# Performance work log

Hardware: AMD Instinct MI355X
Metric: run time of the kernel (lower is better)

The kernel has to match this reference:

```python
import jax, jax.numpy as jnp
import numpy as np

N_NODES = 30000
N_REL = 8
N_EDGES = 150000
EMB = 128
HID = 128
OUT = 256
HEADS = 4
RANK = 8
SCALE = 1.0
NEG_SLOPE = 0.2
LN_EPS = 1e-5


def setup_inputs():
    key = jax.random.key(0)
    ks = jax.random.split(key, 16)
    def nrm(k, shp, s=0.05):
        return jax.random.normal(k, shp, dtype=jnp.float32) * s
    d2 = HEADS * HID  # conv2 input dim = 512
    return {
        "entity_emb": nrm(ks[0], (N_NODES, EMB)),
        "A1": nrm(ks[1], (N_REL, EMB * RANK)),
        "B1": nrm(ks[2], (N_REL, EMB * RANK)),
        "W1": nrm(ks[3], (HEADS * HID, EMB)),
        "att_l1": nrm(ks[4], (1, HEADS, HID)),
        "att_r1": nrm(ks[5], (1, HEADS, HID)),
        "relb1": jnp.zeros((N_REL, HEADS), jnp.float32),
        "bias1": jnp.zeros((HEADS * HID,), jnp.float32),
        "A2": nrm(ks[6], (N_REL, d2 * RANK)),
        "B2": nrm(ks[7], (N_REL, d2 * RANK)),
        "W2": nrm(ks[8], (OUT, d2)),
        "att_l2": nrm(ks[9], (1, 1, OUT)),
        "att_r2": nrm(ks[10], (1, 1, OUT)),
        "relb2": jnp.zeros((N_REL, 1), jnp.float32),
        "bias2": jnp.zeros((OUT,), jnp.float32),
        "res_W": nrm(ks[11], (OUT, EMB)),
        "res_b": jnp.zeros((OUT,), jnp.float32),
        "ln_g": jnp.ones((OUT,), jnp.float32),
        "ln_b": jnp.zeros((OUT,), jnp.float32),
        "edge_index": jax.random.randint(ks[12], (2, N_EDGES), 0, N_NODES),
        "edge_type": jax.random.randint(ks[13], (N_EDGES,), 0, N_REL),
    }


def _rel_gat_conv(x, A, B, W, att_l, att_r, relb, bias, j_idx, i_idx, etype, heads, out_dim, concat):
    # x: [N,d]; A,B: [R, d*k]; W: [heads*out_dim, d]
    N, d = x.shape
    R = A.shape[0]
    k = RANK
    HC = heads * out_dim
    A3 = A.reshape(R, d, k)
    B3 = B.reshape(R, d, k)
    z_all = x @ W.T  # [N, HC] base linear (shared by z_i and z_j)
    # LoRA low-rank projection per (node, relation): P[n,r] = B_r^T x_n
    P = jnp.einsum('nd,rdk->nrk', x, B3)          # [N,R,k] (small)
    low = P[j_idx, etype]                          # [E,k]
    # Fused LoRA-through-lin: lin(scale*A_r B_r^T x) = scale * low @ (A_r^T W^T)
    M = jnp.einsum('rdk,hd->rkh', A3, W).reshape(R * k, HC)  # [R*k, HC]
    oh = jax.nn.one_hot(etype, R, dtype=x.dtype)   # [E,R]
    low_exp = (oh[:, :, None] * low[:, None, :]).reshape(-1, R * k)  # [E,R*k]
    z_j = (z_all[j_idx] + SCALE * (low_exp @ M)).reshape(-1, heads, out_dim)  # [E,H,C]
    z_i = z_all[i_idx].reshape(-1, heads, out_dim)                            # [E,H,C]
    alpha = (z_i * att_l).sum(-1) + (z_j * att_r).sum(-1) + relb[etype]       # [E,H]
    alpha = jax.nn.leaky_relu(alpha, NEG_SLOPE)
    # per-relation loop => softmax groups are (relation, target node)
    seg = etype * N + i_idx
    n_seg = R * N
    amax = jax.ops.segment_max(alpha, seg, num_segments=n_seg)
    ex = jnp.exp(alpha - amax[seg])
    den = jax.ops.segment_sum(ex, seg, num_segments=n_seg)
    alpha = ex / den[seg]
    msg = z_j * alpha[:, :, None]                  # [E,H,C]
    out = jax.ops.segment_sum(msg, i_idx, num_segments=N)  # [N,H,C]
    out = out.reshape(N, HC) if concat else out.mean(axis=1)
    return out + bias


def _forward(entity_emb, A1, B1, W1, att_l1, att_r1, relb1, bias1,
             A2, B2, W2, att_l2, att_r2, relb2, bias2,
             res_W, res_b, ln_g, ln_b, edge_index, edge_type):
    j_idx, i_idx = edge_index[0], edge_index[1]
    x0 = entity_emb
    x = _rel_gat_conv(x0, A1, B1, W1, att_l1, att_r1, relb1, bias1,
                      j_idx, i_idx, edge_type, HEADS, HID, True)
    x = jax.nn.elu(x)
    x = _rel_gat_conv(x, A2, B2, W2, att_l2, att_r2, relb2, bias2,
                      j_idx, i_idx, edge_type, 1, OUT, False)
    x = x + (x0 @ res_W.T + res_b)
    mu = x.mean(axis=-1, keepdims=True)
    var = ((x - mu) ** 2).mean(axis=-1, keepdims=True)
    return (x - mu) / jnp.sqrt(var + LN_EPS) * ln_g + ln_b


def reference(entity_emb, A1, B1, W1, att_l1, att_r1, relb1, bias1,
              A2, B2, W2, att_l2, att_r2, relb2, bias2,
              res_W, res_b, ln_g, ln_b, edge_index, edge_type):
    return _forward(entity_emb, A1, B1, W1, att_l1, att_r1, relb1, bias1,
                    A2, B2, W2, att_l2, att_r2, relb2, bias2,
                    res_W, res_b, ln_g, ln_b, edge_index, edge_type)
```

## Files before the change

kernel.cpp:

```cpp
#include <hip/hip_runtime.h>
#include <cstddef>

#define NRELS 8
#define EMB 128
#define HID 128
#define OUTD 256
#define HEADS 4
#define RANK 8
#define D2 512
#define KCAT 192
#define NEG_SLOPE 0.2f
#define LN_EPS 1e-5f

typedef short bf16x8 __attribute__((ext_vector_type(8)));
typedef float f32x4 __attribute__((ext_vector_type(4)));

__device__ __forceinline__ unsigned short f2bf(float f) {
  union { float f; unsigned u; } v; v.f = f;
  unsigned u = v.u;
  return (unsigned short)((u + 0x7fffu + ((u >> 16) & 1u)) >> 16);
}
__device__ __forceinline__ float bf2f(unsigned short u) {
  union { unsigned u; float f; } v; v.u = (unsigned)u << 16; return v.f;
}

#define GLOAD16(ldsp, gp) \
  __builtin_amdgcn_global_load_lds((const __attribute__((address_space(1))) unsigned int*)(gp), \
      (__attribute__((address_space(3))) unsigned int*)(ldsp), 16, 0, 0)

template<int BIAS, int F32OUT, int ELU, int PB>
__global__ __launch_bounds__(256) void gemm_tile(const unsigned short* __restrict__ A,
    const unsigned short* __restrict__ B, unsigned short* __restrict__ C,
    float* __restrict__ Cf, const unsigned short* __restrict__ Bp,
    float* __restrict__ Cp, int M, int N, int K, int lda, int aoffc,
    const float* __restrict__ bias, const float* __restrict__ b1p) {
  __shared__ unsigned short As[2][128 * 32];
  __shared__ unsigned short Bs[2][128 * 32];
  const int tid = threadIdx.x;
  const int wave = tid >> 6;
  const int lane = tid & 63;
  const int wm = wave & 1;
  const int wn = wave >> 1;
  const int r16 = lane & 15;
  const int quad = lane >> 4;
  const int bm = blockIdx.x * 128;
  const int lr = lane >> 2;
  const int lc = ((lane & 3) ^ ((lane >> 3) & 3)) * 8;
  const int rsw = (quad ^ ((r16 >> 1) & 3)) * 8;
  const bool isP = PB && (blockIdx.y == (int)gridDim.y - 1);
  const unsigned short* Bu = isP ? Bp : B;
  const int bn = isP ? 0 : blockIdx.y * 128;
  const unsigned short* Abase = A + (size_t)blockIdx.y * (isP ? 0 : aoffc);
  int ar0 = bm + wave * 32 + lr;      if (ar0 >= M) ar0 = M - 1;
  int ar1 = bm + wave * 32 + 16 + lr; if (ar1 >= M) ar1 = M - 1;
  const unsigned short* Ag0 = Abase + (size_t)ar0 * lda + lc;
  const unsigned short* Ag1 = Abase + (size_t)ar1 * lda + lc;
  const unsigned short* Bg0 = Bu + (size_t)(bn + wave * 32 + lr) * K + lc;
  const unsigned short* Bg1 = Bu + (size_t)(bn + wave * 32 + 16 + lr) * K + lc;
  f32x4 acc[4][4] = {};
  GLOAD16(As[0] + wave * 1024, Ag0);
  GLOAD16(As[0] + wave * 1024 + 512, Ag1);
  GLOAD16(Bs[0] + wave * 1024, Bg0);
  GLOAD16(Bs[0] + wave * 1024 + 512, Bg1);
  __syncthreads();
  int cur = 0;
  for (int k0 = 0; k0 < K; k0 += 32) {
    if (k0 + 32 < K) {
      GLOAD16(As[cur ^ 1] + wave * 1024, Ag0 + k0 + 32);
      GLOAD16(As[cur ^ 1] + wave * 1024 + 512, Ag1 + k0 + 32);
      GLOAD16(Bs[cur ^ 1] + wave * 1024, Bg0 + k0 + 32);
      GLOAD16(Bs[cur ^ 1] + wave * 1024 + 512, Bg1 + k0 + 32);
    }
    bf16x8 af[4], bfr[4];
#pragma unroll
    for (int mi = 0; mi < 4; ++mi)
      af[mi] = *(const bf16x8*)(As[cur] + (wm * 64 + mi * 16 + r16) * 32 + rsw);
#pragma unroll
    for (int ni = 0; ni < 4; ++ni)
      bfr[ni] = *(const bf16x8*)(Bs[cur] + (wn * 64 + ni * 16 + r16) * 32 + rsw);
#pragma unroll
    for (int mi = 0; mi < 4; ++mi)
#pragma unroll
      for (int ni = 0; ni < 4; ++ni)
        acc[mi][ni] = __builtin_amdgcn_mfma_f32_16x16x32_bf16(af[mi], bfr[ni], acc[mi][ni], 0, 0, 0);
    __syncthreads();
    cur ^= 1;
  }
  float bcol[4];
  if (BIAS) {
#pragma unroll
    for (int ni = 0; ni < 4; ++ni) {
      int cn = bn + wn * 64 + ni * 16 + r16;
      bcol[ni] = bias[cn];
      if (F32OUT) bcol[ni] += b1p[cn];
    }
  }
#pragma unroll
  for (int mi = 0; mi < 4; ++mi)
#pragma unroll
    for (int ni = 0; ni < 4; ++ni)
#pragma unroll
      for (int r = 0; r < 4; ++r) {
        int row = bm + wm * 64 + mi * 16 + quad * 4 + r;
        if (row < M) {
          int col = wn * 64 + ni * 16 + r16;
          float v = acc[mi][ni][r];
          if (isP) {
            Cp[(size_t)row * 128 + col] = v;
          } else {
            if (BIAS) v += bcol[ni];
            if (ELU) v = v > 0.f ? v : expm1f(v);
            size_t idx = (size_t)row * N + bn + col;
            if (F32OUT) Cf[idx] = v;
            else        C[idx] = f2bf(v);
          }
        }
      }
}

__global__ __launch_bounds__(256) void gemm_abt2(const float* __restrict__ Amat1,
    const float* __restrict__ W1, float* __restrict__ M1o,
    const float* __restrict__ Amat2, const float* __restrict__ W2, float* __restrict__ M2o) {
  const float* A; const float* B; float* C; int N, K, bn;
  if (blockIdx.x < D2 / 64) { A = Amat1; B = W1; C = M1o; N = D2; K = EMB; bn = blockIdx.x * 64; }
  else { A = Amat2; B = W2; C = M2o; N = OUTD; K = D2; bn = (blockIdx.x - D2 / 64) * 64; }
  __shared__ float As[32][64];
  __shared__ float Bs[32][64];
  const int tid = threadIdx.x;
  const int tx = tid & 15;
  const int ty = tid >> 4;
  const int lr = tid & 63;
  const int lq = tid >> 6;
  float acc[4][4] = {};
  for (int k0 = 0; k0 < K; k0 += 32) {
#pragma unroll
    for (int s = 0; s < 2; ++s) {
      const int q = lq + s * 4;
      float4 va = *(const float4*)(A + (size_t)lr * K + k0 + q * 4);
      As[q * 4 + 0][lr] = va.x; As[q * 4 + 1][lr] = va.y;
      As[q * 4 + 2][lr] = va.z; As[q * 4 + 3][lr] = va.w;
      float4 vb = *(const float4*)(B + (size_t)(bn + lr) * K + k0 + q * 4);
      Bs[q * 4 + 0][lr] = vb.x; Bs[q * 4 + 1][lr] = vb.y;
      Bs[q * 4 + 2][lr] = vb.z; Bs[q * 4 + 3][lr] = vb.w;
    }
    __syncthreads();
#pragma unroll
    for (int kk = 0; kk < 32; ++kk) {
      float a[4], b[4];
#pragma unroll
      for (int i2 = 0; i2 < 4; ++i2) { a[i2] = As[kk][ty * 4 + i2]; b[i2] = Bs[kk][tx * 4 + i2]; }
#pragma unroll
      for (int i2 = 0; i2 < 4; ++i2)
#pragma unroll
        for (int j2 = 0; j2 < 4; ++j2)
          acc[i2][j2] = fmaf(a[i2], b[j2], acc[i2][j2]);
    }
    __syncthreads();
  }
#pragma unroll
  for (int i2 = 0; i2 < 4; ++i2)
#pragma unroll
    for (int j2 = 0; j2 < 4; ++j2)
      C[(size_t)(ty * 4 + i2) * N + bn + tx * 4 + j2] = acc[i2][j2];
}

__global__ void prep_all(const float* __restrict__ x0, const float* __restrict__ W2,
    const float* __restrict__ res_W,
    const float* __restrict__ A1, const float* __restrict__ A2,
    const float* __restrict__ B1, const float* __restrict__ B2,
    unsigned short* __restrict__ x0b, unsigned short* __restrict__ Acat,
    unsigned short* __restrict__ W2b, unsigned short* __restrict__ RWcat,
    float* __restrict__ Amat1, float* __restrict__ Amat2,
    unsigned short* __restrict__ Bmat1b, unsigned short* __restrict__ Bmat2b,
    const int* __restrict__ ii, int* __restrict__ ideg, int* __restrict__ prepos,
    int E, int nx0) {
  int idx = blockIdx.x * 256 + threadIdx.x;
  if (idx < E) { prepos[idx] = atomicAdd(&ideg[ii[idx]], 1); return; } idx -= E;
  if (idx < nx0) { unsigned short b = f2bf(x0[idx]); x0b[idx] = b;
    Acat[(size_t)(idx >> 7) * KCAT + (idx & 127)] = b; return; } idx -= nx0;
  if (idx < OUTD * D2) { W2b[idx] = f2bf(W2[idx]); return; } idx -= OUTD * D2;
  if (idx < OUTD * EMB) { RWcat[(size_t)(idx >> 7) * KCAT + (idx & 127)] = f2bf(res_W[idx]); return; } idx -= OUTD * EMB;
  if (idx < 64 * EMB) { int d = idx % EMB, rk = idx / EMB, k = rk & 7, r = rk >> 3;
    Amat1[idx] = A1[(size_t)r * EMB * RANK + (size_t)d * RANK + k]; return; } idx -= 64 * EMB;
  if (idx < 64 * D2) { int d = idx % D2, rk = idx / D2, k = rk & 7, r = rk >> 3;
    Amat2[idx] = A2[(size_t)r * D2 * RANK + (size_t)d * RANK + k]; return; } idx -= 64 * D2;
  if (idx < 64 * EMB) { int d = idx % EMB, rk = idx / EMB, k = rk & 7, r = rk >> 3;
    Bmat1b[idx] = f2bf(B1[(size_t)r * EMB * RANK + (size_t)d * RANK + k]); return; } idx -= 64 * EMB;
  if (idx < 64 * D2) { int d = idx % D2, rk = idx / D2, k = rk & 7, r = rk >> 3;
    Bmat2b[idx] = f2bf(B2[(size_t)r * D2 * RANK + (size_t)d * RANK + k]); }
}

__global__ void fold_build(const float* __restrict__ M1, const float* __restrict__ M2,
    const float* __restrict__ W1, const float* __restrict__ W2,
    const float* __restrict__ attL1, const float* __restrict__ attR1,
    const float* __restrict__ attL2, const float* __restrict__ attR2,
    const unsigned short* __restrict__ Bmat1b, const unsigned short* __restrict__ Bmat2b,
    unsigned short* __restrict__ Bcat1, unsigned short* __restrict__ RWcat,
    unsigned short* __restrict__ Bp1ext, unsigned short* __restrict__ Bp2ext,
    float* __restrict__ Matt1, float* __restrict__ Matt2) {
  int idx = blockIdx.x * 256 + threadIdx.x;
  if (idx < 512 * 192) { int c = idx / 192, t = idx % 192;
    float v = (t < 128) ? W1[(size_t)c * EMB + t] : M1[(size_t)(t - 128) * D2 + c];
    Bcat1[idx] = f2bf(v); return; } idx -= 512 * 192;
  if (idx < 256 * 64) { int c = idx >> 6, rk = idx & 63;
    RWcat[(size_t)c * KCAT + 128 + rk] = f2bf(M2[(size_t)rk * OUTD + c]); return; } idx -= 256 * 64;
  if (idx < 128 * 128) { int r = idx >> 7, d = idx & 127;
    unsigned short v;
    if (r < 64) v = Bmat1b[r * 128 + d];
    else if (r < 72) { int h = (r - 64) & 3;
      const float* att = (r < 68) ? attL1 : attR1;
      float s = 0.f;
      for (int c = 0; c < HID; ++c)
        s = fmaf(W1[(size_t)(h * HID + c) * EMB + d], att[h * HID + c], s);
      v = f2bf(s); }
    else v = 0;
    Bp1ext[idx] = v; return; } idx -= 128 * 128;
  if (idx < 128 * 512) { int r = idx >> 9, d = idx & 511;
    unsigned short v;
    if (r < 64) v = Bmat2b[r * 512 + d];
    else if (r < 66) { const float* att = (r == 64) ? attL2 : attR2;
      float s = 0.f;
      for (int c = 0; c < OUTD; ++c)
        s = fmaf(W2[(size_t)c * D2 + d], att[c], s);
      v = f2bf(s); }
    else v = 0;
    Bp2ext[idx] = v; return; } idx -= 128 * 512;
  if (idx < 256) { int h = idx & 3, rk = idx >> 2;
    float s = 0.f;
    for (int c = 0; c < HID; ++c)
      s = fmaf(M1[(size_t)rk * D2 + h * HID + c], attR1[h * HID + c], s);
    Matt1[rk * 4 + h] = s; return; } idx -= 256;
  if (idx < 64) {
    float s = 0.f;
    for (int c = 0; c < OUTD; ++c) s = fmaf(M2[(size_t)idx * OUTD + c], attR2[c], s);
    Matt2[idx] = s; }
}

__global__ __launch_bounds__(1024) void exscan_kernel(const int* __restrict__ deg,
                                                      int* __restrict__ rowstart, int n) {
  __shared__ int wsum[16];
  int t = threadIdx.x;
  int lane = t & 63, wid = t >> 6;
  int carry = 0;
  for (int base = 0; base < n; base += 4096) {
    int i0 = base + t * 4;
    int v0 = 0, v1 = 0, v2 = 0, v3 = 0;
    if (i0 + 3 < n) {
      int4 vv = *(const int4*)(deg + i0);
      v0 = vv.x; v1 = vv.y; v2 = vv.z; v3 = vv.w;
    } else {
      if (i0 < n) v0 = deg[i0];
      if (i0 + 1 < n) v1 = deg[i0 + 1];
      if (i0 + 2 < n) v2 = deg[i0 + 2];
      if (i0 + 3 < n) v3 = deg[i0 + 3];
    }
    int tot = v0 + v1 + v2 + v3;
    int x = tot;
#pragma unroll
    for (int o = 1; o < 64; o <<= 1) {
      int y = __shfl_up(x, o, 64);
      if (lane >= o) x += y;
    }
    if (lane == 63) wsum[wid] = x;
    __syncthreads();
    if (t == 0) {
      int s = carry;
      for (int w2 = 0; w2 < 16; ++w2) { int tmp = wsum[w2]; wsum[w2] = s; s += tmp; }
      carry = s;
    }
    __syncthreads();
    int ex0 = x - tot + wsum[wid];
    if (i0 + 3 < n) {
      int4 ov; ov.x = ex0; ov.y = ex0 + v0; ov.z = ex0 + v0 + v1; ov.w = ex0 + v0 + v1 + v2;
      *(int4*)(rowstart + i0) = ov;
    } else {
      if (i0 < n) rowstart[i0] = ex0;
      if (i0 + 1 < n) rowstart[i0 + 1] = ex0 + v0;
      if (i0 + 2 < n) rowstart[i0 + 2] = ex0 + v0 + v1;
      if (i0 + 3 < n) rowstart[i0 + 3] = ex0 + v0 + v1 + v2;
    }
    __syncthreads();
  }
  if (t == 0) rowstart[n] = carry;
}

__global__ void edge_alpha1(const int* __restrict__ ji, const int* __restrict__ ii,
                            const int* __restrict__ et, const int* __restrict__ rowstart,
                            const int* __restrict__ prepos,
                            const float* __restrict__ Cp1,
                            const float* __restrict__ relb1, const float* __restrict__ Matt1,
                            float4* __restrict__ recs1, int E) {
  int e = blockIdx.x * blockDim.x + threadIdx.x;
  if (e >= E) return;
  int j = ji[e], i = ii[e], rt = et[e];
  float4 lo0 = *(const float4*)(Cp1 + (size_t)j * 128 + rt * 8);
  float4 lo1 = *(const float4*)(Cp1 + (size_t)j * 128 + rt * 8 + 4);
  float low[RANK] = {lo0.x, lo0.y, lo0.z, lo0.w, lo1.x, lo1.y, lo1.z, lo1.w};
  float4 ali = *(const float4*)(Cp1 + (size_t)i * 128 + 64);
  float4 arj = *(const float4*)(Cp1 + (size_t)j * 128 + 68);
  float4 rb  = *(const float4*)(relb1 + rt * 4);
  float a0 = ali.x + arj.x + rb.x;
  float a1 = ali.y + arj.y + rb.y;
  float a2 = ali.z + arj.z + rb.z;
  float a3 = ali.w + arj.w + rb.w;
#pragma unroll
  for (int k = 0; k < RANK; ++k) {
    float4 mk = *(const float4*)(Matt1 + ((rt * 8 + k) << 2));
    a0 = fmaf(low[k], mk.x, a0); a1 = fmaf(low[k], mk.y, a1);
    a2 = fmaf(low[k], mk.z, a2); a3 = fmaf(low[k], mk.w, a3);
  }
  a0 = (a0 > 0.f) ? a0 : NEG_SLOPE * a0;
  a1 = (a1 > 0.f) ? a1 : NEG_SLOPE * a1;
  a2 = (a2 > 0.f) ? a2 : NEG_SLOPE * a2;
  a3 = (a3 > 0.f) ? a3 : NEG_SLOPE * a3;
  float e0 = expf(a0), e1 = expf(a1), e2 = expf(a2), e3 = expf(a3);
  float4* rp = recs1 + (size_t)(rowstart[i] + prepos[e]) * 4;
  rp[0] = make_float4(__int_as_float(j), e0, e1, e2);
  rp[1] = make_float4(e3, __int_as_float(rt), low[0], low[1]);
  rp[2] = make_float4(low[2], low[3], low[4], low[5]);
  rp[3] = make_float4(low[6], low[7], 0.f, 0.f);
}

__global__ __launch_bounds__(256) void agg1f(const float4* __restrict__ recs1,
    const int* __restrict__ rowstart, const unsigned short* __restrict__ x0b,
    unsigned short* __restrict__ XQ1, int Nn) {
  __shared__ float denS[4][32];
  const int wid = threadIdx.x >> 6, lane = threadIdx.x & 63;
  const int i = blockIdx.x * 4 + wid;
  if (i >= Nn) return;
  const int rt_mine = lane >> 3, k = lane & 7;
  const int s0 = rowstart[i], deg = rowstart[i + 1] - s0;
  const float* rf = (const float*)recs1;
  const size_t xb = (size_t)i * 768;
  {
    float q0 = 0.f, q1 = 0.f, q2 = 0.f, q3 = 0.f;
    float d0 = 0.f, d1 = 0.f, d2 = 0.f, d3 = 0.f;
    float4 a0 = {}, a1 = {};
    float lw = 0.f;
    if (deg > 0) {
      a0 = recs1[(size_t)s0 * 4]; a1 = recs1[(size_t)s0 * 4 + 1];
      lw = rf[(size_t)s0 * 16 + 6 + k];
    }
    for (int p = 0; p < deg; ++p) {
      float4 b0 = a0, b1 = a1; float lwn = lw;
      if (p + 1 < deg) {
        b0 = recs1[(size_t)(s0 + p + 1) * 4]; b1 = recs1[(size_t)(s0 + p + 1) * 4 + 1];
        lwn = rf[(size_t)(s0 + p + 1) * 16 + 6 + k];
      }
      int rt = __float_as_int(a1.y);
      if (rt == rt_mine) {
        q0 = fmaf(a0.y, lw, q0); q1 = fmaf(a0.z, lw, q1);
        q2 = fmaf(a0.w, lw, q2); q3 = fmaf(a1.x, lw, q3);
        d0 += a0.y; d1 += a0.z; d2 += a0.w; d3 += a1.x;
      }
      a0 = b0; a1 = b1; lw = lwn;
    }
    float r0 = (d0 > 0.f) ? 1.f / d0 : 0.f;
    float r1 = (d1 > 0.f) ? 1.f / d1 : 0.f;
    float r2 = (d2 > 0.f) ? 1.f / d2 : 0.f;
    float r3 = (d3 > 0.f) ? 1.f / d3 : 0.f;
    XQ1[xb + 0 * 192 + 128 + lane] = f2bf(q0 * r0);
    XQ1[xb + 1 * 192 + 128 + lane] = f2bf(q1 * r1);
    XQ1[xb + 2 * 192 + 128 + lane] = f2bf(q2 * r2);
    XQ1[xb + 3 * 192 + 128 + lane] = f2bf(q3 * r3);
    if (k == 0) {
      denS[wid][rt_mine]      = r0;
      denS[wid][8 + rt_mine]  = r1;
      denS[wid][16 + rt_mine] = r2;
      denS[wid][24 + rt_mine] = r3;
    }
  }
  const int c0 = lane * 2;
  float acc[8] = {};
  float4 r0 = {}, r1 = {};
  float2 g0 = {}, g1 = {};
  unsigned za = 0u, zn0 = 0u;
  if (deg > 0) { r0 = recs1[(size_t)s0 * 4]; g0 = *(const float2*)(rf + (size_t)s0 * 16 + 4);
    za = *(const unsigned*)(x0b + (size_t)__float_as_int(r0.x) * 128 + c0); }
  if (deg > 1) { r1 = recs1[(size_t)(s0 + 1) * 4]; g1 = *(const float2*)(rf + (size_t)(s0 + 1) * 16 + 4); }
  for (int p = 0; p < deg; ++p) {
    float4 r2 = r1; float2 g2 = g1; unsigned zb = za;
    if (p + 2 < deg) { r2 = recs1[(size_t)(s0 + p + 2) * 4];
                       g2 = *(const float2*)(rf + (size_t)(s0 + p + 2) * 16 + 4); }
    if (p + 1 < deg) zb = *(const unsigned*)(x0b + (size_t)__float_as_int(r1.x) * 128 + c0);
    int rt = __float_as_int(g0.y);
    float w0 = r0.y * denS[wid][rt];
    float w1 = r0.z * denS[wid][8 + rt];
    float w2 = r0.w * denS[wid][16 + rt];
    float w3 = g0.x * denS[wid][24 + rt];
    float v0 = bf2f((unsigned short)(za & 0xffff));
    float v1 = bf2f((unsigned short)(za >> 16));
    acc[0] = fmaf(w0, v0, acc[0]); acc[1] = fmaf(w0, v1, acc[1]);
    acc[2] = fmaf(w1, v0, acc[2]); acc[3] = fmaf(w1, v1, acc[3]);
    acc[4] = fmaf(w2, v0, acc[4]); acc[5] = fmaf(w2, v1, acc[5]);
    acc[6] = fmaf(w3, v0, acc[6]); acc[7] = fmaf(w3, v1, acc[7]);
    r0 = r1; g0 = g1; r1 = r2; g1 = g2; za = zb;
  }
#pragma unroll
  for (int h = 0; h < 4; ++h) {
    unsigned pv = (unsigned)f2bf(acc[2 * h]) | ((unsigned)f2bf(acc[2 * h + 1]) << 16);
    *(unsigned*)(XQ1 + xb + h * 192 + c0) = pv;
  }
}

__global__ void edge_alpha2(const int* __restrict__ ji, const int* __restrict__ ii,
                            const int* __restrict__ et, const int* __restrict__ rowstart,
                            const int* __restrict__ prepos,
                            const float* __restrict__ Cp2,
                            const float* __restrict__ relb2, const float* __restrict__ Matt2,
                            float4* __restrict__ recs2, int E) {
  int e = blockIdx.x * blockDim.x + threadIdx.x;
  if (e >= E) return;
  int j = ji[e], i = ii[e], rt = et[e];
  float4 lo0 = *(const float4*)(Cp2 + (size_t)j * 128 + rt * 8);
  float4 lo1 = *(const float4*)(Cp2 + (size_t)j * 128 + rt * 8 + 4);
  float low[RANK] = {lo0.x, lo0.y, lo0.z, lo0.w, lo1.x, lo1.y, lo1.z, lo1.w};
  float a = Cp2[(size_t)i * 128 + 64] + Cp2[(size_t)j * 128 + 65] + relb2[rt];
#pragma unroll
  for (int k = 0; k < RANK; ++k) a = fmaf(low[k], Matt2[rt * RANK + k], a);
  a = (a > 0.f) ? a : NEG_SLOPE * a;
  float ex = expf(a);
  float4* rp = recs2 + (size_t)(rowstart[i] + prepos[e]) * 3;
  rp[0] = make_float4(__int_as_float(j), __int_as_float(rt), ex, low[0]);
  rp[1] = make_float4(low[1], low[2], low[3], low[4]);
  rp[2] = make_float4(low[5], low[6], low[7], 0.f);
}

__global__ __launch_bounds__(256) void qden2(const float4* __restrict__ recs2,
    const int* __restrict__ rowstart, unsigned short* __restrict__ Acat,
    float* __restrict__ rden2, int Nn) {
  const int wid = threadIdx.x >> 6, lane = threadIdx.x & 63;
  const int i = blockIdx.x * 4 + wid;
  if (i >= Nn) return;
  const int rt_mine = lane >> 3, k = lane & 7;
  const int s0 = rowstart[i], deg = rowstart[i + 1] - s0;
  const float* rf = (const float*)recs2;
  float q = 0.f, d = 0.f;
  float4 a0 = {}; float lw = 0.f;
  if (deg > 0) { a0 = recs2[(size_t)s0 * 3]; lw = rf[(size_t)s0 * 12 + 3 + k]; }
  for (int p = 0; p < deg; ++p) {
    float4 b0 = a0; float lwn = lw;
    if (p + 1 < deg) {
      b0 = recs2[(size_t)(s0 + p + 1) * 3];
      lwn = rf[(size_t)(s0 + p + 1) * 12 + 3 + k];
    }
    int rt = __float_as_int(a0.y);
    if (rt == rt_mine) { q = fmaf(a0.z, lw, q); d += a0.z; }
    a0 = b0; lw = lwn;
  }
  float rd = (d > 0.f) ? 1.f / d : 0.f;
  Acat[(size_t)i * KCAT + 128 + lane] = f2bf(q * rd);
  if (k == 0) rden2[(size_t)i * 8 + rt_mine] = rd;
}

__global__ __launch_bounds__(256) void node_agg2_lite(const float4* __restrict__ recs2,
    const int* __restrict__ rowstart, const unsigned short* __restrict__ z2b,
    const float* __restrict__ rden2, const float* __restrict__ o2,
    const float* __restrict__ ln_g, const float* __restrict__ ln_b,
    float* __restrict__ y, int Nn) {
  const int wid = threadIdx.x >> 6;
  const int lane = threadIdx.x & 63;
  const int i = blockIdx.x * 4 + wid;
  if (i >= Nn) return;
  __shared__ float denS[4][NRELS];
  if (lane < NRELS) denS[wid][lane] = rden2[(size_t)i * 8 + lane];
  const int s0 = rowstart[i];
  const int deg = rowstart[i + 1] - s0;
  const int c0 = lane * 4;
  float acc[4] = {};
  float4 r0 = {}, r1 = {}, r2 = {};
  uint2 za = make_uint2(0u, 0u), zb = make_uint2(0u, 0u);
  if (deg > 0) { r0 = recs2[(size_t)s0 * 3];
    za = *(const uint2*)(z2b + (size_t)__float_as_int(r0.x) * OUTD + c0); }
  if (deg > 1) { r1 = recs2[(size_t)(s0 + 1) * 3];
    zb = *(const uint2*)(z2b + (size_t)__float_as_int(r1.x) * OUTD + c0); }
  if (deg > 2) r2 = recs2[(size_t)(s0 + 2) * 3];
  for (int p = 0; p < deg; ++p) {
    float4 r3 = r2;
    uint2 zn = zb;
    if (p + 3 < deg) r3 = recs2[(size_t)(s0 + p + 3) * 3];
    if (p + 2 < deg)
      zn = *(const uint2*)(z2b + (size_t)__float_as_int(r2.x) * OUTD + c0);
    int rt = __float_as_int(r0.y);
    float wt = r0.z * denS[wid][rt];
    acc[0] = fmaf(wt, bf2f((unsigned short)(za.x & 0xffff)), acc[0]);
    acc[1] = fmaf(wt, bf2f((unsigned short)(za.x >> 16)), acc[1]);
    acc[2] = fmaf(wt, bf2f((unsigned short)(za.y & 0xffff)), acc[2]);
    acc[3] = fmaf(wt, bf2f((unsigned short)(za.y >> 16)), acc[3]);
    r0 = r1; r1 = r2; r2 = r3; za = zb; zb = zn;
  }
  float4 rsv = *(const float4*)(o2 + (size_t)i * OUTD + c0);
  float vv[4];
  vv[0] = acc[0] + rsv.x;
  vv[1] = acc[1] + rsv.y;
  vv[2] = acc[2] + rsv.z;
  vv[3] = acc[3] + rsv.w;
  float s = vv[0] + vv[1] + vv[2] + vv[3];
  for (int o = 32; o > 0; o >>= 1) s += __shfl_xor(s, o, 64);
  float mu = s * (1.f / OUTD);
  float q = 0.f;
#pragma unroll
  for (int k = 0; k < 4; ++k) { float d = vv[k] - mu; q += d * d; }
  for (int o = 32; o > 0; o >>= 1) q += __shfl_xor(q, o, 64);
  float rstd = rsqrtf(q * (1.f / OUTD) + LN_EPS);
  float4 g = *(const float4*)(ln_g + c0);
  float4 bb = *(const float4*)(ln_b + c0);
  float4 ov;
  ov.x = (vv[0] - mu) * rstd * g.x + bb.x;
  ov.y = (vv[1] - mu) * rstd * g.y + bb.y;
  ov.z = (vv[2] - mu) * rstd * g.z + bb.z;
  ov.w = (vv[3] - mu) * rstd * g.w + bb.w;
  *(float4*)(y + (size_t)i * OUTD + c0) = ov;
}

extern "C" void kernel_launch(void* const* d_in, const int* in_sizes, int n_in,
                              void* d_out, int out_size, void* d_ws, size_t ws_size,
                              hipStream_t stream) {
  const float* x0     = (const float*)d_in[0];
  const float* A1     = (const float*)d_in[1];
  const float* B1     = (const float*)d_in[2];
  const float* W1     = (const float*)d_in[3];
  const float* attL1  = (const float*)d_in[4];
  const float* attR1  = (const float*)d_in[5];
  const float* relb1  = (const float*)d_in[6];
  const float* bias1  = (const float*)d_in[7];
  const float* A2     = (const float*)d_in[8];
  const float* B2     = (const float*)d_in[9];
  const float* W2     = (const float*)d_in[10];
  const float* attL2  = (const float*)d_in[11];
  const float* attR2  = (const float*)d_in[12];
  const float* relb2  = (const float*)d_in[13];
  const float* bias2  = (const float*)d_in[14];
  const float* res_W  = (const float*)d_in[15];
  const float* res_b  = (const float*)d_in[16];
  const float* ln_g   = (const float*)d_in[17];
  const float* ln_b   = (const float*)d_in[18];
  const int*   eidx   = (const int*)d_in[19];
  const int*   etype  = (const int*)d_in[20];
  float* out = (float*)d_out;

  const int Nn = in_sizes[0] / EMB;
  const int E  = in_sizes[20];
  const int* ji = eidx;
  const int* ii = eidx + E;

  float* w = (float*)d_ws;
  size_t off = 0;
  float* o2    = w + off; off += (size_t)Nn * OUTD;
  float* Cp1   = w + off; off += (size_t)Nn * 128;
  float* Cp2   = w + off; off += (size_t)Nn * 128;
  float* M1    = w + off; off += 64 * D2;
  float* M2    = w + off; off += 64 * OUTD;
  float* Amat1 = w + off; off += 64 * EMB;
  float* Amat2 = w + off; off += 64 * D2;
  float* Matt1 = w + off; off += 64 * 4;
  float* Matt2 = w + off; off += 64;
  float* rden2 = w + off; off += (size_t)Nn * 8;
  float4* recs1 = (float4*)(w + off); off += (size_t)E * 16;
  float4* recs2 = (float4*)(w + off); off += (size_t)E * 12;
  unsigned short* z2b    = (unsigned short*)(w + off); off += (size_t)Nn * OUTD / 2;
  unsigned short* x0b    = (unsigned short*)(w + off); off += (size_t)Nn * EMB / 2;
  unsigned short* h1b    = (unsigned short*)(w + off); off += (size_t)Nn * D2 / 2;
  unsigned short* XQ1    = (unsigned short*)(w + off); off += (size_t)Nn * 768 / 2;
  unsigned short* W2b    = (unsigned short*)(w + off); off += (size_t)OUTD * D2 / 2;
  unsigned short* Bmat1b = (unsigned short*)(w + off); off += (size_t)64 * EMB / 2;
  unsigned short* Bmat2b = (unsigned short*)(w + off); off += (size_t)64 * D2 / 2;
  unsigned short* Acat   = (unsigned short*)(w + off); off += (size_t)Nn * KCAT / 2;
  unsigned short* RWcat  = (unsigned short*)(w + off); off += (size_t)OUTD * KCAT / 2;
  unsigned short* Bcat1  = (unsigned short*)(w + off); off += (size_t)512 * 192 / 2;
  unsigned short* Bp1ext = (unsigned short*)(w + off); off += (size_t)128 * 128 / 2;
  unsigned short* Bp2ext = (unsigned short*)(w + off); off += (size_t)128 * 512 / 2;
  int* ideg     = (int*)(w + off); off += (size_t)Nn;
  int* prepos   = (int*)(w + off); off += (size_t)E;
  int* rowstart = (int*)(w + off); off += (size_t)Nn + 1;
  (void)ws_size; (void)n_in; (void)out_size;

  const int MT128 = (Nn + 127) / 128;
  const int NB4 = (Nn + 3) / 4;

  (void)hipMemsetAsync(ideg, 0, (size_t)Nn * sizeof(int), stream);
  {
    int nx0 = Nn * EMB;
    int total = E + nx0 + OUTD * D2 + OUTD * EMB + 64 * EMB + 64 * D2 + 64 * EMB + 64 * D2;
    prep_all<<<(total + 255) / 256, 256, 0, stream>>>(x0, W2, res_W, A1, A2, B1, B2,
        x0b, Acat, W2b, RWcat, Amat1, Amat2, Bmat1b, Bmat2b, ii, ideg, prepos, E, nx0);
  }
  exscan_kernel<<<1, 1024, 0, stream>>>(ideg, rowstart, Nn);

  gemm_abt2<<<dim3(D2 / 64 + OUTD / 64, 1), 256, 0, stream>>>(Amat1, W1, M1, Amat2, W2, M2);
  {
    int total = 512 * 192 + 256 * 64 + 128 * 128 + 128 * 512 + 256 + 64;
    fold_build<<<(total + 255) / 256, 256, 0, stream>>>(M1, M2, W1, W2, attL1, attR1,
        attL2, attR2, Bmat1b, Bmat2b, Bcat1, RWcat, Bp1ext, Bp2ext, Matt1, Matt2);
  }

  gemm_tile<0, 1, 0, 0><<<dim3(MT128, 1), 256, 0, stream>>>(x0b, Bp1ext, nullptr, Cp1,
      nullptr, nullptr, Nn, 128, EMB, EMB, 0, nullptr, nullptr);

  edge_alpha1<<<(E + 255) / 256, 256, 0, stream>>>(ji, ii, etype, rowstart, prepos, Cp1,
                                                   relb1, Matt1, recs1, E);
  agg1f<<<NB4, 256, 0, stream>>>(recs1, rowstart, x0b, XQ1, Nn);
  gemm_tile<1, 0, 1, 0><<<dim3(MT128, 4), 256, 0, stream>>>(XQ1, Bcat1, h1b, nullptr,
      nullptr, nullptr, Nn, D2, 192, 768, 192, bias1, nullptr);

  gemm_tile<0, 0, 0, 1><<<dim3(MT128, 3), 256, 0, stream>>>(h1b, W2b, z2b, nullptr,
      Bp2ext, Cp2, Nn, OUTD, D2, D2, 0, nullptr, nullptr);

  edge_alpha2<<<(E + 255) / 256, 256, 0, stream>>>(ji, ii, etype, rowstart, prepos, Cp2,
                                                   relb2, Matt2, recs2, E);
  qden2<<<NB4, 256, 0, stream>>>(recs2, rowstart, Acat, rden2, Nn);
  gemm_tile<1, 1, 0, 0><<<dim3(MT128, 2), 256, 0, stream>>>(Acat, RWcat, nullptr, o2,
      nullptr, nullptr, Nn, OUTD, KCAT, KCAT, 0, bias2, res_b);
  node_agg2_lite<<<NB4, 256, 0, stream>>>(recs2, rowstart, z2b, rden2, o2, ln_g, ln_b, out, Nn);
}
```

Measured before the change: 341.5 us.

## Merge prep-stage kernels and pack edge records into bf16 compact format

Several small setup kernels are folded into fewer launches. The weight-fold GEMM now runs alongside the x0 projection GEMM in one grid, the fold-build runs alongside edge_alpha1, and the Matt computation runs inside the scan kernel, now reassociated as Amat·(W^T att). Edge records are repacked: relation type and source index share one word, and the low-rank values are stored as bf16 pairs, which shrinks recs1 and recs2. This is meant to cut launch count and edge-record memory traffic, at the cost of lower precision on the LoRA terms and extra unpack work in the gather loops.

Result: no change. 341.1 us (-0.1%).

```diff
diff --git a/kernel.cpp b/kernel.cpp
--- a/kernel.cpp
+++ b/kernel.cpp
@@ -11,6 +11,7 @@
 #define KCAT 192
 #define NEG_SLOPE 0.2f
 #define LN_EPS 1e-5f
+#define JMASK 0x07FFFFFFu
 
 typedef short bf16x8 __attribute__((ext_vector_type(8)));
 typedef float f32x4 __attribute__((ext_vector_type(4)));
@@ -23,19 +24,23 @@
 __device__ __forceinline__ float bf2f(unsigned short u) {
   union { unsigned u; float f; } v; v.u = (unsigned)u << 16; return v.f;
 }
+__device__ __forceinline__ unsigned pk2(float a, float b) {
+  return (unsigned)f2bf(a) | ((unsigned)f2bf(b) << 16);
+}
+__device__ __forceinline__ unsigned asu(float f) { return __float_as_uint(f); }
 
 #define GLOAD16(ldsp, gp) \
   __builtin_amdgcn_global_load_lds((const __attribute__((address_space(1))) unsigned int*)(gp), \
       (__attribute__((address_space(3))) unsigned int*)(ldsp), 16, 0, 0)
 
 template<int BIAS, int F32OUT, int ELU, int PB>
-__global__ __launch_bounds__(256) void gemm_tile(const unsigned short* __restrict__ A,
-    const unsigned short* __restrict__ B, unsigned short* __restrict__ C,
-    float* __restrict__ Cf, const unsigned short* __restrict__ Bp,
-    float* __restrict__ Cp, int M, int N, int K, int lda, int aoffc,
+__device__ __forceinline__ void gemm_tile_body(unsigned short* AsB, unsigned short* BsB,
+    int bx, int by, int ny,
+    const unsigned short* __restrict__ A, const unsigned short* __restrict__ B,
+    unsigned short* __restrict__ C, float* __restrict__ Cf,
+    const unsigned short* __restrict__ Bp, float* __restrict__ Cp,
+    int M, int N, int K, int lda, int aoffc,
     const float* __restrict__ bias, const float* __restrict__ b1p) {
-  __shared__ unsigned short As[2][128 * 32];
-  __shared__ unsigned short Bs[2][128 * 32];
   const int tid = threadIdx.x;
   const int wave = tid >> 6;
   const int lane = tid & 63;
@@ -43,14 +48,14 @@
   const int wn = wave >> 1;
   const int r16 = lane & 15;
   const int quad = lane >> 4;
-  const int bm = blockIdx.x * 128;
+  const int bm = bx * 128;
   const int lr = lane >> 2;
   const int lc = ((lane & 3) ^ ((lane >> 3) & 3)) * 8;
   const int rsw = (quad ^ ((r16 >> 1) & 3)) * 8;
-  const bool isP = PB && (blockIdx.y == (int)gridDim.y - 1);
+  const bool isP = PB && (by == ny - 1);
   const unsigned short* Bu = isP ? Bp : B;
-  const int bn = isP ? 0 : blockIdx.y * 128;
-  const unsigned short* Abase = A + (size_t)blockIdx.y * (isP ? 0 : aoffc);
+  const int bn = isP ? 0 : by * 128;
+  const unsigned short* Abase = A + (size_t)by * (isP ? 0 : aoffc);
   int ar0 = bm + wave * 32 + lr;      if (ar0 >= M) ar0 = M - 1;
   int ar1 = bm + wave * 32 + 16 + lr; if (ar1 >= M) ar1 = M - 1;
   const unsigned short* Ag0 = Abase + (size_t)ar0 * lda + lc;
@@ -58,26 +63,26 @@
   const unsigned short* Bg0 = Bu + (size_t)(bn + wave * 32 + lr) * K + lc;
   const unsigned short* Bg1 = Bu + (size_t)(bn + wave * 32 + 16 + lr) * K + lc;
   f32x4 acc[4][4] = {};
-  GLOAD16(As[0] + wave * 1024, Ag0);
-  GLOAD16(As[0] + wave * 1024 + 512, Ag1);
-  GLOAD16(Bs[0] + wave * 1024, Bg0);
-  GLOAD16(Bs[0] + wave * 1024 + 512, Bg1);
+  GLOAD16(AsB + wave * 1024, Ag0);
+  GLOAD16(AsB + wave * 1024 + 512, Ag1);
+  GLOAD16(BsB + wave * 1024, Bg0);
+  GLOAD16(BsB + wave * 1024 + 512, Bg1);
   __syncthreads();
   int cur = 0;
   for (int k0 = 0; k0 < K; k0 += 32) {
     if (k0 + 32 < K) {
-      GLOAD16(As[cur ^ 1] + wave * 1024, Ag0 + k0 + 32);
-      GLOAD16(As[cur ^ 1] + wave * 1024 + 512, Ag1 + k0 + 32);
-      GLOAD16(Bs[cur ^ 1] + wave * 1024, Bg0 + k0 + 32);
-      GLOAD16(Bs[cur ^ 1] + wave * 1024 + 512, Bg1 + k0 + 32);
+      GLOAD16(AsB + (cur ^ 1) * 4096 + wave * 1024, Ag0 + k0 + 32);
+      GLOAD16(AsB + (cur ^ 1) * 4096 + wave * 1024 + 512, Ag1 + k0 + 32);
+      GLOAD16(BsB + (cur ^ 1) * 4096 + wave * 1024, Bg0 + k0 + 32);
+      GLOAD16(BsB + (cur ^ 1) * 4096 + wave * 1024 + 512, Bg1 + k0 + 32);
     }
     bf16x8 af[4], bfr[4];
 #pragma unroll
     for (int mi = 0; mi < 4; ++mi)
-      af[mi] = *(const bf16x8*)(As[cur] + (wm * 64 + mi * 16 + r16) * 32 + rsw);
+      af[mi] = *(const bf16x8*)(AsB + cur * 4096 + (wm * 64 + mi * 16 + r16) * 32 + rsw);
 #pragma unroll
     for (int ni = 0; ni < 4; ++ni)
-      bfr[ni] = *(const bf16x8*)(Bs[cur] + (wn * 64 + ni * 16 + r16) * 32 + rsw);
+      bfr[ni] = *(const bf16x8*)(BsB + cur * 4096 + (wn * 64 + ni * 16 + r16) * 32 + rsw);
 #pragma unroll
     for (int mi = 0; mi < 4; ++mi)
 #pragma unroll
@@ -118,60 +123,86 @@
       }
 }
 
-__global__ __launch_bounds__(256) void gemm_abt2(const float* __restrict__ Amat1,
+template<int BIAS, int F32OUT, int ELU, int PB>
+__global__ __launch_bounds__(256) void gemm_tile(const unsigned short* __restrict__ A,
+    const unsigned short* __restrict__ B, unsigned short* __restrict__ C,
+    float* __restrict__ Cf, const unsigned short* __restrict__ Bp,
+    float* __restrict__ Cp, int M, int N, int K, int lda, int aoffc,
+    const float* __restrict__ bias, const float* __restrict__ b1p) {
+  __shared__ unsigned short As[2 * 4096];
+  __shared__ unsigned short Bs[2 * 4096];
+  gemm_tile_body<BIAS, F32OUT, ELU, PB>(As, Bs, blockIdx.x, blockIdx.y, gridDim.y,
+      A, B, C, Cf, Bp, Cp, M, N, K, lda, aoffc, bias, b1p);
+}
+
+__global__ __launch_bounds__(256) void combo_abt_p1(const float* __restrict__ Amat1,
     const float* __restrict__ W1, float* __restrict__ M1o,
-    const float* __restrict__ Amat2, const float* __restrict__ W2, float* __restrict__ M2o) {
-  const float* A; const float* B; float* C; int N, K, bn;
-  if (blockIdx.x < D2 / 64) { A = Amat1; B = W1; C = M1o; N = D2; K = EMB; bn = blockIdx.x * 64; }
-  else { A = Amat2; B = W2; C = M2o; N = OUTD; K = D2; bn = (blockIdx.x - D2 / 64) * 64; }
-  __shared__ float As[32][64];
-  __shared__ float Bs[32][64];
-  const int tid = threadIdx.x;
-  const int tx = tid & 15;
-  const int ty = tid >> 4;
-  const int lr = tid & 63;
-  const int lq = tid >> 6;
-  float acc[4][4] = {};
-  for (int k0 = 0; k0 < K; k0 += 32) {
-#pragma unroll
-    for (int s = 0; s < 2; ++s) {
-      const int q = lq + s * 4;
-      float4 va = *(const float4*)(A + (size_t)lr * K + k0 + q * 4);
-      As[q * 4 + 0][lr] = va.x; As[q * 4 + 1][lr] = va.y;
-      As[q * 4 + 2][lr] = va.z; As[q * 4 + 3][lr] = va.w;
-      float4 vb = *(const float4*)(B + (size_t)(bn + lr) * K + k0 + q * 4);
-      Bs[q * 4 + 0][lr] = vb.x; Bs[q * 4 + 1][lr] = vb.y;
-      Bs[q * 4 + 2][lr] = vb.z; Bs[q * 4 + 3][lr] = vb.w;
-    }
-    __syncthreads();
-#pragma unroll
-    for (int kk = 0; kk < 32; ++kk) {
-      float a[4], b[4];
-#pragma unroll
-      for (int i2 = 0; i2 < 4; ++i2) { a[i2] = As[kk][ty * 4 + i2]; b[i2] = Bs[kk][tx * 4 + i2]; }
-#pragma unroll
-      for (int i2 = 0; i2 < 4; ++i2)
-#pragma unroll
-        for (int j2 = 0; j2 < 4; ++j2)
-          acc[i2][j2] = fmaf(a[i2], b[j2], acc[i2][j2]);
-    }
-    __syncthreads();
-  }
-#pragma unroll
-  for (int i2 = 0; i2 < 4; ++i2)
-#pragma unroll
-    for (int j2 = 0; j2 < 4; ++j2)
-      C[(size_t)(ty * 4 + i2) * N + bn + tx * 4 + j2] = acc[i2][j2];
-}
-
-__global__ void prep_all(const float* __restrict__ x0, const float* __restrict__ W2,
-    const float* __restrict__ res_W,
+    const float* __restrict__ Amat2, const float* __restrict__ W2, float* __restrict__ M2o,
+    const unsigned short* __restrict__ x0b, const unsigned short* __restrict__ Bp1ext,
+    float* __restrict__ Cp1, int Nn) {
+  __shared__ unsigned short GA[2 * 4096];
+  __shared__ unsigned short GB[2 * 4096];
+  const int bx = blockIdx.x;
+  if (bx < 12) {
+    float* As_ = (float*)GA;
+    float* Bs_ = (float*)GB;
+    const float* A; const float* B; float* C; int N, K, bn;
+    if (bx < 8) { A = Amat1; B = W1; C = M1o; N = D2; K = EMB; bn = bx * 64; }
+    else { A = Amat2; B = W2; C = M2o; N = OUTD; K = D2; bn = (bx - 8) * 64; }
+    const int tid = threadIdx.x;
+    const int tx = tid & 15;
+    const int ty = tid >> 4;
+    const int lr2 = tid & 63;
+    const int lq = tid >> 6;
+    float acc[4][4] = {};
+    for (int k0 = 0; k0 < K; k0 += 32) {
+#pragma unroll
+      for (int s = 0; s < 2; ++s) {
+        const int q = lq + s * 4;
+        float4 va = *(const float4*)(A + (size_t)lr2 * K + k0 + q * 4);
+        As_[(q * 4 + 0) * 64 + lr2] = va.x; As_[(q * 4 + 1) * 64 + lr2] = va.y;
+        As_[(q * 4 + 2) * 64 + lr2] = va.z; As_[(q * 4 + 3) * 64 + lr2] = va.w;
+        float4 vb = *(const float4*)(B + (size_t)(bn + lr2) * K + k0 + q * 4);
+        Bs_[(q * 4 + 0) * 64 + lr2] = vb.x; Bs_[(q * 4 + 1) * 64 + lr2] = vb.y;
+        Bs_[(q * 4 + 2) * 64 + lr2] = vb.z; Bs_[(q * 4 + 3) * 64 + lr2] = vb.w;
+      }
+      __syncthreads();
+#pragma unroll
+      for (int kk = 0; kk < 32; ++kk) {
+        float a[4], b[4];
+#pragma unroll
+        for (int i2 = 0; i2 < 4; ++i2) { a[i2] = As_[kk * 64 + ty * 4 + i2]; b[i2] = Bs_[kk * 64 + tx * 4 + i2]; }
+#pragma unroll
+        for (int i2 = 0; i2 < 4; ++i2)
+#pragma unroll
+          for (int j2 = 0; j2 < 4; ++j2)
+            acc[i2][j2] = fmaf(a[i2], b[j2], acc[i2][j2]);
+      }
+      __syncthreads();
+    }
+#pragma unroll
+    for (int i2 = 0; i2 < 4; ++i2)
+#pragma unroll
+      for (int j2 = 0; j2 < 4; ++j2)
+        C[(size_t)(ty * 4 + i2) * N + bn + tx * 4 + j2] = acc[i2][j2];
+  } else {
+    gemm_tile_body<0, 1, 0, 0>(GA, GB, bx - 12, 0, 1, x0b, Bp1ext, nullptr, Cp1,
+                               nullptr, nullptr, Nn, 128, EMB, EMB, 0, nullptr, nullptr);
+  }
+}
+
+__global__ void prep_all(const float* __restrict__ x0, const float* __restrict__ W1,
+    const float* __restrict__ W2, const float* __restrict__ res_W,
     const float* __restrict__ A1, const float* __restrict__ A2,
     const float* __restrict__ B1, const float* __restrict__ B2,
+    const float* __restrict__ attL1, const float* __restrict__ attR1,
+    const float* __restrict__ attL2, const float* __restrict__ attR2,
     unsigned short* __restrict__ x0b, unsigned short* __restrict__ Acat,
     unsigned short* __restrict__ W2b, unsigned short* __restrict__ RWcat,
     float* __restrict__ Amat1, float* __restrict__ Amat2,
-    unsigned short* __restrict__ Bmat1b, unsigned short* __restrict__ Bmat2b,
+    unsigned short* __restrict__ Bp1ext, unsigned short* __restrict__ Bp2ext,
+    unsigned short* __restrict__ Bcat1,
+    float* __restrict__ awR1f, float* __restrict__ awR2f,
     const int* __restrict__ ii, int* __restrict__ ideg, int* __restrict__ prepos,
     int E, int nx0) {
   int idx = blockIdx.x * 256 + threadIdx.x;
@@ -185,76 +216,77 @@
   if (idx < 64 * D2) { int d = idx % D2, rk = idx / D2, k = rk & 7, r = rk >> 3;
     Amat2[idx] = A2[(size_t)r * D2 * RANK + (size_t)d * RANK + k]; return; } idx -= 64 * D2;
   if (idx < 64 * EMB) { int d = idx % EMB, rk = idx / EMB, k = rk & 7, r = rk >> 3;
-    Bmat1b[idx] = f2bf(B1[(size_t)r * EMB * RANK + (size_t)d * RANK + k]); return; } idx -= 64 * EMB;
+    Bp1ext[idx] = f2bf(B1[(size_t)r * EMB * RANK + (size_t)d * RANK + k]); return; } idx -= 64 * EMB;
   if (idx < 64 * D2) { int d = idx % D2, rk = idx / D2, k = rk & 7, r = rk >> 3;
-    Bmat2b[idx] = f2bf(B2[(size_t)r * D2 * RANK + (size_t)d * RANK + k]); }
-}
-
-__global__ void fold_build(const float* __restrict__ M1, const float* __restrict__ M2,
-    const float* __restrict__ W1, const float* __restrict__ W2,
-    const float* __restrict__ attL1, const float* __restrict__ attR1,
-    const float* __restrict__ attL2, const float* __restrict__ attR2,
-    const unsigned short* __restrict__ Bmat1b, const unsigned short* __restrict__ Bmat2b,
-    unsigned short* __restrict__ Bcat1, unsigned short* __restrict__ RWcat,
-    unsigned short* __restrict__ Bp1ext, unsigned short* __restrict__ Bp2ext,
-    float* __restrict__ Matt1, float* __restrict__ Matt2) {
-  int idx = blockIdx.x * 256 + threadIdx.x;
-  if (idx < 512 * 192) { int c = idx / 192, t = idx % 192;
-    float v = (t < 128) ? W1[(size_t)c * EMB + t] : M1[(size_t)(t - 128) * D2 + c];
-    Bcat1[idx] = f2bf(v); return; } idx -= 512 * 192;
-  if (idx < 256 * 64) { int c = idx >> 6, rk = idx & 63;
-    RWcat[(size_t)c * KCAT + 128 + rk] = f2bf(M2[(size_t)rk * OUTD + c]); return; } idx -= 256 * 64;
-  if (idx < 128 * 128) { int r = idx >> 7, d = idx & 127;
-    unsigned short v;
-    if (r < 64) v = Bmat1b[r * 128 + d];
-    else if (r < 72) { int h = (r - 64) & 3;
-      const float* att = (r < 68) ? attL1 : attR1;
-      float s = 0.f;
-      for (int c = 0; c < HID; ++c)
-        s = fmaf(W1[(size_t)(h * HID + c) * EMB + d], att[h * HID + c], s);
-      v = f2bf(s); }
-    else v = 0;
-    Bp1ext[idx] = v; return; } idx -= 128 * 128;
-  if (idx < 128 * 512) { int r = idx >> 9, d = idx & 511;
-    unsigned short v;
-    if (r < 64) v = Bmat2b[r * 512 + d];
-    else if (r < 66) { const float* att = (r == 64) ? attL2 : attR2;
-      float s = 0.f;
-      for (int c = 0; c < OUTD; ++c)
-        s = fmaf(W2[(size_t)c * D2 + d], att[c], s);
-      v = f2bf(s); }
-    else v = 0;
-    Bp2ext[idx] = v; return; } idx -= 128 * 512;
-  if (idx < 256) { int h = idx & 3, rk = idx >> 2;
+    Bp2ext[idx] = f2bf(B2[(size_t)r * D2 * RANK + (size_t)d * RANK + k]); return; } idx -= 64 * D2;
+  if (idx < 1024) {
+    int rr = idx >> 7, d = idx & 127;
+    int h = rr & 3; bool isL = rr < 4;
+    const float* att = isL ? attL1 : attR1;
     float s = 0.f;
     for (int c = 0; c < HID; ++c)
-      s = fmaf(M1[(size_t)rk * D2 + h * HID + c], attR1[h * HID + c], s);
-    Matt1[rk * 4 + h] = s; return; } idx -= 256;
-  if (idx < 64) {
+      s = fmaf(W1[(size_t)(h * HID + c) * EMB + d], att[h * HID + c], s);
+    Bp1ext[(64 + rr) * 128 + d] = f2bf(s);
+    if (!isL) awR1f[h * 128 + d] = s;
+    return; } idx -= 1024;
+  if (idx < 1024) {
+    int rr = idx >> 9, d = idx & 511;
+    const float* att = (rr == 0) ? attL2 : attR2;
     float s = 0.f;
-    for (int c = 0; c < OUTD; ++c) s = fmaf(M2[(size_t)idx * OUTD + c], attR2[c], s);
-    Matt2[idx] = s; }
-}
-
-__global__ __launch_bounds__(1024) void exscan_kernel(const int* __restrict__ deg,
-                                                      int* __restrict__ rowstart, int n) {
+    for (int c = 0; c < OUTD; ++c)
+      s = fmaf(W2[(size_t)c * D2 + d], att[c], s);
+    Bp2ext[(size_t)(64 + rr) * 512 + d] = f2bf(s);
+    if (rr == 1) awR2f[d] = s;
+    return; } idx -= 1024;
+  if (idx < 56 * 128) { Bp1ext[72 * 128 + idx] = 0; return; } idx -= 56 * 128;
+  if (idx < 62 * 512) { Bp2ext[66 * 512 + idx] = 0; return; } idx -= 62 * 512;
+  if (idx < 512 * 128) { int c = idx >> 7, t = idx & 127;
+    Bcat1[(size_t)c * KCAT + t] = f2bf(W1[(size_t)c * EMB + t]); }
+}
+
+__global__ __launch_bounds__(1024) void exscan_matt(const int* __restrict__ deg,
+    int* __restrict__ rowstart, int n,
+    const float* __restrict__ Amat1, const float* __restrict__ awR1f, float* __restrict__ Matt1,
+    const float* __restrict__ Amat2, const float* __restrict__ awR2f, float* __restrict__ Matt2) {
+  if (blockIdx.x == 1) {
+    int t = threadIdx.x;
+    if (t < 256) {
+      int rk = t >> 2, h = t & 3;
+      float s = 0.f;
+      for (int d = 0; d < 128; ++d)
+        s = fmaf(Amat1[rk * 128 + d], awR1f[h * 128 + d], s);
+      Matt1[t] = s;
+    }
+    return;
+  }
+  if (blockIdx.x == 2) {
+    int t = threadIdx.x;
+    if (t < 64) {
+      float s = 0.f;
+      for (int d = 0; d < 512; ++d) s = fmaf(Amat2[t * 512 + d], awR2f[d], s);
+      Matt2[t] = s;
+    }
+    return;
+  }
   __shared__ int wsum[16];
   int t = threadIdx.x;
   int lane = t & 63, wid = t >> 6;
   int carry = 0;
-  for (int base = 0; base < n; base += 4096) {
-    int i0 = base + t * 4;
-    int v0 = 0, v1 = 0, v2 = 0, v3 = 0;
-    if (i0 + 3 < n) {
-      int4 vv = *(const int4*)(deg + i0);
-      v0 = vv.x; v1 = vv.y; v2 = vv.z; v3 = vv.w;
+  for (int base = 0; base < n; base += 8192) {
+    int i0 = base + t * 8;
+    int v[8];
+    if (i0 + 7 < n) {
+      int4 a = *(const int4*)(deg + i0);
+      int4 b = *(const int4*)(deg + i0 + 4);
+      v[0] = a.x; v[1] = a.y; v[2] = a.z; v[3] = a.w;
+      v[4] = b.x; v[5] = b.y; v[6] = b.z; v[7] = b.w;
     } else {
-      if (i0 < n) v0 = deg[i0];
-      if (i0 + 1 < n) v1 = deg[i0 + 1];
-      if (i0 + 2 < n) v2 = deg[i0 + 2];
-      if (i0 + 3 < n) v3 = deg[i0 + 3];
-    }
-    int tot = v0 + v1 + v2 + v3;
+#pragma unroll
+      for (int q = 0; q < 8; ++q) v[q] = (i0 + q < n) ? deg[i0 + q] : 0;
+    }
+    int tot = 0;
+#pragma unroll
+    for (int q = 0; q < 8; ++q) tot += v[q];
     int x = tot;
 #pragma unroll
     for (int o = 1; o < 64; o <<= 1) {
@@ -270,27 +302,35 @@
     }
     __syncthreads();
     int ex0 = x - tot + wsum[wid];
-    if (i0 + 3 < n) {
-      int4 ov; ov.x = ex0; ov.y = ex0 + v0; ov.z = ex0 + v0 + v1; ov.w = ex0 + v0 + v1 + v2;
-      *(int4*)(rowstart + i0) = ov;
-    } else {
-      if (i0 < n) rowstart[i0] = ex0;
-      if (i0 + 1 < n) rowstart[i0 + 1] = ex0 + v0;
-      if (i0 + 2 < n) rowstart[i0 + 2] = ex0 + v0 + v1;
-      if (i0 + 3 < n) rowstart[i0 + 3] = ex0 + v0 + v1 + v2;
+#pragma unroll
+    for (int q = 0; q < 8; ++q) {
+      if (i0 + q < n) rowstart[i0 + q] = ex0;
+      ex0 += v[q];
     }
     __syncthreads();
   }
   if (t == 0) rowstart[n] = carry;
 }
 
-__global__ void edge_alpha1(const int* __restrict__ ji, const int* __restrict__ ii,
-                            const int* __restrict__ et, const int* __restrict__ rowstart,
-                            const int* __restrict__ prepos,
-                            const float* __restrict__ Cp1,
-                            const float* __restrict__ relb1, const float* __restrict__ Matt1,
-                            float4* __restrict__ recs1, int E) {
-  int e = blockIdx.x * blockDim.x + threadIdx.x;
+#define FB_BLOCKS 192
+__global__ void combo_fold_ea1(const float* __restrict__ M1, const float* __restrict__ M2,
+    unsigned short* __restrict__ Bcat1, unsigned short* __restrict__ RWcat,
+    const int* __restrict__ ji, const int* __restrict__ ii,
+    const int* __restrict__ et, const int* __restrict__ rowstart,
+    const int* __restrict__ prepos, const float* __restrict__ Cp1,
+    const float* __restrict__ relb1, const float* __restrict__ Matt1,
+    float4* __restrict__ recs1, int E) {
+  const int bx = blockIdx.x;
+  if (bx < FB_BLOCKS) {
+    int idx = bx * 256 + threadIdx.x;
+    if (idx < 512 * 64) { int c = idx >> 6, rk = idx & 63;
+      Bcat1[(size_t)c * KCAT + 128 + rk] = f2bf(M1[(size_t)rk * D2 + c]); return; }
+    idx -= 512 * 64;
+    if (idx < 256 * 64) { int c = idx >> 6, rk = idx & 63;
+      RWcat[(size_t)c * KCAT + 128 + rk] = f2bf(M2[(size_t)rk * OUTD + c]); }
+    return;
+  }
+  int e = (bx - FB_BLOCKS) * 256 + threadIdx.x;
   if (e >= E) return;
   int j = ji[e], i = ii[e], rt = et[e];
   float4 lo0 = *(const float4*)(Cp1 + (size_t)j * 128 + rt * 8);
@@ -314,11 +354,13 @@
   a2 = (a2 > 0.f) ? a2 : NEG_SLOPE * a2;
   a3 = (a3 > 0.f) ? a3 : NEG_SLOPE * a3;
   float e0 = expf(a0), e1 = expf(a1), e2 = expf(a2), e3 = expf(a3);
-  float4* rp = recs1 + (size_t)(rowstart[i] + prepos[e]) * 4;
-  rp[0] = make_float4(__int_as_float(j), e0, e1, e2);
-  rp[1] = make_float4(e3, __int_as_float(rt), low[0], low[1]);
-  rp[2] = make_float4(low[2], low[3], low[4], low[5]);
-  rp[3] = make_float4(low[6], low[7], 0.f, 0.f);
+  unsigned pack = ((unsigned)rt << 27) | (unsigned)j;
+  float4* rp = recs1 + (size_t)(rowstart[i] + prepos[e]) * 3;
+  rp[0] = make_float4(__uint_as_float(pack), e0, e1, e2);
+  rp[1] = make_float4(e3, __uint_as_float(pk2(low[0], low[1])),
+                      __uint_as_float(pk2(low[2], low[3])),
+                      __uint_as_float(pk2(low[4], low[5])));
+  rp[2] = make_float4(__uint_as_float(pk2(low[6], low[7])), 0.f, 0.f, 0.f);
 }
 
 __global__ __launch_bounds__(256) void agg1f(const float4* __restrict__ recs1,
@@ -336,24 +378,28 @@
     float q0 = 0.f, q1 = 0.f, q2 = 0.f, q3 = 0.f;
     float d0 = 0.f, d1 = 0.f, d2 = 0.f, d3 = 0.f;
     float4 a0 = {}, a1 = {};
-    float lw = 0.f;
+    float a2x = 0.f;
     if (deg > 0) {
-      a0 = recs1[(size_t)s0 * 4]; a1 = recs1[(size_t)s0 * 4 + 1];
-      lw = rf[(size_t)s0 * 16 + 6 + k];
-    }
+      a0 = recs1[(size_t)s0 * 3]; a1 = recs1[(size_t)s0 * 3 + 1];
+      a2x = rf[(size_t)s0 * 12 + 8];
+    }
+    const int sel = k >> 1;
     for (int p = 0; p < deg; ++p) {
-      float4 b0 = a0, b1 = a1; float lwn = lw;
+      float4 b0 = a0, b1 = a1; float b2x = a2x;
       if (p + 1 < deg) {
-        b0 = recs1[(size_t)(s0 + p + 1) * 4]; b1 = recs1[(size_t)(s0 + p + 1) * 4 + 1];
-        lwn = rf[(size_t)(s0 + p + 1) * 16 + 6 + k];
+        b0 = recs1[(size_t)(s0 + p + 1) * 3]; b1 = recs1[(size_t)(s0 + p + 1) * 3 + 1];
+        b2x = rf[(size_t)(s0 + p + 1) * 12 + 8];
       }
-      int rt = __float_as_int(a1.y);
+      int rt = (int)(asu(a0.x) >> 27);
       if (rt == rt_mine) {
+        float pw = (sel == 0) ? a1.y : (sel == 1) ? a1.z : (sel == 2) ? a1.w : a2x;
+        unsigned pu = asu(pw);
+        float lw = bf2f((unsigned short)((k & 1) ? (pu >> 16) : (pu & 0xffff)));
         q0 = fmaf(a0.y, lw, q0); q1 = fmaf(a0.z, lw, q1);
         q2 = fmaf(a0.w, lw, q2); q3 = fmaf(a1.x, lw, q3);
         d0 += a0.y; d1 += a0.z; d2 += a0.w; d3 += a1.x;
       }
-      a0 = b0; a1 = b1; lw = lwn;
+      a0 = b0; a1 = b1; a2x = b2x;
     }
     float r0 = (d0 > 0.f) ? 1.f / d0 : 0.f;
     float r1 = (d1 > 0.f) ? 1.f / d1 : 0.f;
@@ -373,32 +419,32 @@
   const int c0 = lane * 2;
   float acc[8] = {};
   float4 r0 = {}, r1 = {};
-  float2 g0 = {}, g1 = {};
-  unsigned za = 0u, zn0 = 0u;
-  if (deg > 0) { r0 = recs1[(size_t)s0 * 4]; g0 = *(const float2*)(rf + (size_t)s0 * 16 + 4);
-    za = *(const unsigned*)(x0b + (size_t)__float_as_int(r0.x) * 128 + c0); }
-  if (deg > 1) { r1 = recs1[(size_t)(s0 + 1) * 4]; g1 = *(const float2*)(rf + (size_t)(s0 + 1) * 16 + 4); }
+  float e30 = 0.f, e31 = 0.f;
+  unsigned za = 0u;
+  if (deg > 0) { r0 = recs1[(size_t)s0 * 3]; e30 = rf[(size_t)s0 * 12 + 4];
+    za = *(const unsigned*)(x0b + (size_t)(asu(r0.x) & JMASK) * 128 + c0); }
+  if (deg > 1) { r1 = recs1[(size_t)(s0 + 1) * 3]; e31 = rf[(size_t)(s0 + 1) * 12 + 4]; }
   for (int p = 0; p < deg; ++p) {
-    float4 r2 = r1; float2 g2 = g1; unsigned zb = za;
-    if (p + 2 < deg) { r2 = recs1[(size_t)(s0 + p + 2) * 4];
-                       g2 = *(const float2*)(rf + (size_t)(s0 + p + 2) * 16 + 4); }
-    if (p + 1 < deg) zb = *(const unsigned*)(x0b + (size_t)__float_as_int(r1.x) * 128 + c0);
-    int rt = __float_as_int(g0.y);
+    float4 r2 = r1; float e32 = e31; unsigned zb = za;
+    if (p + 2 < deg) { r2 = recs1[(size_t)(s0 + p + 2) * 3];
+                       e32 = rf[(size_t)(s0 + p + 2) * 12 + 4]; }
+    if (p + 1 < deg) zb = *(const unsigned*)(x0b + (size_t)(asu(r1.x) & JMASK) * 128 + c0);
+    int rt = (int)(asu(r0.x) >> 27);
     float w0 = r0.y * denS[wid][rt];
     float w1 = r0.z * denS[wid][8 + rt];
     float w2 = r0.w * denS[wid][16 + rt];
-    float w3 = g0.x * denS[wid][24 + rt];
+    float w3 = e30 * denS[wid][24 + rt];
     float v0 = bf2f((unsigned short)(za & 0xffff));
     float v1 = bf2f((unsigned short)(za >> 16));
     acc[0] = fmaf(w0, v0, acc[0]); acc[1] = fmaf(w0, v1, acc[1]);
     acc[2] = fmaf(w1, v0, acc[2]); acc[3] = fmaf(w1, v1, acc[3]);
     acc[4] = fmaf(w2, v0, acc[4]); acc[5] = fmaf(w2, v1, acc[5]);
     acc[6] = fmaf(w3, v0, acc[6]); acc[7] = fmaf(w3, v1, acc[7]);
-    r0 = r1; g0 = g1; r1 = r2; g1 = g2; za = zb;
+    r0 = r1; e30 = e31; r1 = r2; e31 = e32; za = zb;
   }
 #pragma unroll
   for (int h = 0; h < 4; ++h) {
-    unsigned pv = (unsigned)f2bf(acc[2 * h]) | ((unsigned)f2bf(acc[2 * h + 1]) << 16);
+    unsigned pv = pk2(acc[2 * h], acc[2 * h + 1]);
     *(unsigned*)(XQ1 + xb + h * 192 + c0) = pv;
   }
 }
@@ -420,10 +466,13 @@
   for (int k = 0; k < RANK; ++k) a = fmaf(low[k], Matt2[rt * RANK + k], a);
   a = (a > 0.f) ? a : NEG_SLOPE * a;
   float ex = expf(a);
-  float4* rp = recs2 + (size_t)(rowstart[i] + prepos[e]) * 3;
-  rp[0] = make_float4(__int_as_float(j), __int_as_float(rt), ex, low[0]);
-  rp[1] = make_float4(low[1], low[2], low[3], low[4]);
-  rp[2] = make_float4(low[5], low[6], low[7], 0.f);
+  unsigned pack = ((unsigned)rt << 27) | (unsigned)j;
+  float4* rp = recs2 + (size_t)(rowstart[i] + prepos[e]) * 2;
+  rp[0] = make_float4(__uint_as_float(pack), ex,
+                      __uint_as_float(pk2(low[0], low[1])),
+                      __uint_as_float(pk2(low[2], low[3])));
+  rp[1] = make_float4(__uint_as_float(pk2(low[4], low[5])),
+                      __uint_as_float(pk2(low[6], low[7])), 0.f, 0.f);
 }
 
 __global__ __launch_bounds__(256) void qden2(const float4* __restrict__ recs2,
@@ -436,17 +485,23 @@
   const int s0 = rowstart[i], deg = rowstart[i + 1] - s0;
   const float* rf = (const float*)recs2;
   float q = 0.f, d = 0.f;
-  float4 a0 = {}; float lw = 0.f;
-  if (deg > 0) { a0 = recs2[(size_t)s0 * 3]; lw = rf[(size_t)s0 * 12 + 3 + k]; }
+  float4 a0 = {}; float2 a1 = {};
+  if (deg > 0) { a0 = recs2[(size_t)s0 * 2]; a1 = *(const float2*)(rf + (size_t)s0 * 8 + 4); }
+  const int sel = k >> 1;
   for (int p = 0; p < deg; ++p) {
-    float4 b0 = a0; float lwn = lw;
+    float4 b0 = a0; float2 b1 = a1;
     if (p + 1 < deg) {
-      b0 = recs2[(size_t)(s0 + p + 1) * 3];
-      lwn = rf[(size_t)(s0 + p + 1) * 12 + 3 + k];
-    }
-    int rt = __float_as_int(a0.y);
-    if (rt == rt_mine) { q = fmaf(a0.z, lw, q); d += a0.z; }
-    a0 = b0; lw = lwn;
+      b0 = recs2[(size_t)(s0 + p + 1) * 2];
+      b1 = *(const float2*)(rf + (size_t)(s0 + p + 1) * 8 + 4);
+    }
+    int rt = (int)(asu(a0.x) >> 27);
+    if (rt == rt_mine) {
+      float pw = (sel == 0) ? a0.z : (sel == 1) ? a0.w : (sel == 2) ? a1.x : a1.y;
+      unsigned pu = asu(pw);
+      float lw = bf2f((unsigned short)((k & 1) ? (pu >> 16) : (pu & 0xffff)));
+      q = fmaf(a0.y, lw, q); d += a0.y;
+    }
+    a0 = b0; a1 = b1;
   }
   float rd = (d > 0.f) ? 1.f / d : 0.f;
   Acat[(size_t)i * KCAT + 128 + lane] = f2bf(q * rd);
@@ -470,19 +525,19 @@
   float acc[4] = {};
   float4 r0 = {}, r1 = {}, r2 = {};
   uint2 za = make_uint2(0u, 0u), zb = make_uint2(0u, 0u);
-  if (deg > 0) { r0 = recs2[(size_t)s0 * 3];
-    za = *(const uint2*)(z2b + (size_t)__float_as_int(r0.x) * OUTD + c0); }
-  if (deg > 1) { r1 = recs2[(size_t)(s0 + 1) * 3];
-    zb = *(const uint2*)(z2b + (size_t)__float_as_int(r1.x) * OUTD + c0); }
-  if (deg > 2) r2 = recs2[(size_t)(s0 + 2) * 3];
+  if (deg > 0) { r0 = recs2[(size_t)s0 * 2];
+    za = *(const uint2*)(z2b + (size_t)(asu(r0.x) & JMASK) * OUTD + c0); }
+  if (deg > 1) { r1 = recs2[(size_t)(s0 + 1) * 2];
+    zb = *(const uint2*)(z2b + (size_t)(asu(r1.x) & JMASK) * OUTD + c0); }
+  if (deg > 2) r2 = recs2[(size_t)(s0 + 2) * 2];
   for (int p = 0; p < deg; ++p) {
     float4 r3 = r2;
     uint2 zn = zb;
-    if (p + 3 < deg) r3 = recs2[(size_t)(s0 + p + 3) * 3];
+    if (p + 3 < deg) r3 = recs2[(size_t)(s0 + p + 3) * 2];
     if (p + 2 < deg)
-      zn = *(const uint2*)(z2b + (size_t)__float_as_int(r2.x) * OUTD + c0);
-    int rt = __float_as_int(r0.y);
-    float wt = r0.z * denS[wid][rt];
+      zn = *(const uint2*)(z2b + (size_t)(asu(r2.x) & JMASK) * OUTD + c0);
+    int rt = (int)(asu(r0.x) >> 27);
+    float wt = r0.y * denS[wid][rt];
     acc[0] = fmaf(wt, bf2f((unsigned short)(za.x & 0xffff)), acc[0]);
     acc[1] = fmaf(wt, bf2f((unsigned short)(za.x >> 16)), acc[1]);
     acc[2] = fmaf(wt, bf2f((unsigned short)(za.y & 0xffff)), acc[2]);
@@ -555,19 +610,19 @@
   float* Amat2 = w + off; off += 64 * D2;
   float* Matt1 = w + off; off += 64 * 4;
   float* Matt2 = w + off; off += 64;
+  float* awR1f = w + off; off += 512;
+  float* awR2f = w + off; off += 512;
   float* rden2 = w + off; off += (size_t)Nn * 8;
-  float4* recs1 = (float4*)(w + off); off += (size_t)E * 16;
-  float4* recs2 = (float4*)(w + off); off += (size_t)E * 12;
+  float4* recs1 = (float4*)(w + off); off += (size_t)E * 12;
+  float4* recs2 = (float4*)(w + off); off += (size_t)E * 8;
   unsigned short* z2b    = (unsigned short*)(w + off); off += (size_t)Nn * OUTD / 2;
   unsigned short* x0b    = (unsigned short*)(w + off); off += (size_t)Nn * EMB / 2;
   unsigned short* h1b    = (unsigned short*)(w + off); off += (size_t)Nn * D2 / 2;
   unsigned short* XQ1    = (unsigned short*)(w + off); off += (size_t)Nn * 768 / 2;
   unsigned short* W2b    = (unsigned short*)(w + off); off += (size_t)OUTD * D2 / 2;
-  unsigned short* Bmat1b = (unsigned short*)(w + off); off += (size_t)64 * EMB / 2;
-  unsigned short* Bmat2b = (unsigned short*)(w + off); off += (size_t)64 * D2 / 2;
   unsigned short* Acat   = (unsigned short*)(w + off); off += (size_t)Nn * KCAT / 2;
   unsigned short* RWcat  = (unsigned short*)(w + off); off += (size_t)OUTD * KCAT / 2;
-  unsigned short* Bcat1  = (unsigned short*)(w + off); off += (size_t)512 * 192 / 2;
+  unsigned short* Bcat1  = (unsigned short*)(w + off); off += (size_t)512 * KCAT / 2;
   unsigned short* Bp1ext = (unsigned short*)(w + off); off += (size_t)128 * 128 / 2;
   unsigned short* Bp2ext = (unsigned short*)(w + off); off += (size_t)128 * 512 / 2;
   int* ideg     = (int*)(w + off); off += (size_t)Nn;
@@ -581,27 +636,25 @@
   (void)hipMemsetAsync(ideg, 0, (size_t)Nn * sizeof(int), stream);
   {
     int nx0 = Nn * EMB;
-    int total = E + nx0 + OUTD * D2 + OUTD * EMB + 64 * EMB + 64 * D2 + 64 * EMB + 64 * D2;
-    prep_all<<<(total + 255) / 256, 256, 0, stream>>>(x0, W2, res_W, A1, A2, B1, B2,
-        x0b, Acat, W2b, RWcat, Amat1, Amat2, Bmat1b, Bmat2b, ii, ideg, prepos, E, nx0);
-  }
-  exscan_kernel<<<1, 1024, 0, stream>>>(ideg, rowstart, Nn);
-
-  gemm_abt2<<<dim3(D2 / 64 + OUTD / 64, 1), 256, 0, stream>>>(Amat1, W1, M1, Amat2, W2, M2);
-  {
-    int total = 512 * 192 + 256 * 64 + 128 * 128 + 128 * 512 + 256 + 64;
-    fold_build<<<(total + 255) / 256, 256, 0, stream>>>(M1, M2, W1, W2, attL1, attR1,
-        attL2, attR2, Bmat1b, Bmat2b, Bcat1, RWcat, Bp1ext, Bp2ext, Matt1, Matt2);
-  }
-
-  gemm_tile<0, 1, 0, 0><<<dim3(MT128, 1), 256, 0, stream>>>(x0b, Bp1ext, nullptr, Cp1,
-      nullptr, nullptr, Nn, 128, EMB, EMB, 0, nullptr, nullptr);
-
-  edge_alpha1<<<(E + 255) / 256, 256, 0, stream>>>(ji, ii, etype, rowstart, prepos, Cp1,
-                                                   relb1, Matt1, recs1, E);
+    int total = E + nx0 + OUTD * D2 + OUTD * EMB + 64 * EMB + 64 * D2
+              + 64 * EMB + 64 * D2 + 1024 + 1024 + 56 * 128 + 62 * 512 + 512 * 128;
+    prep_all<<<(total + 255) / 256, 256, 0, stream>>>(x0, W1, W2, res_W, A1, A2, B1, B2,
+        attL1, attR1, attL2, attR2, x0b, Acat, W2b, RWcat, Amat1, Amat2,
+        Bp1ext, Bp2ext, Bcat1, awR1f, awR2f, ii, ideg, prepos, E, nx0);
+  }
+
+  exscan_matt<<<3, 1024, 0, stream>>>(ideg, rowstart, Nn, Amat1, awR1f, Matt1,
+                                      Amat2, awR2f, Matt2);
+
+  combo_abt_p1<<<12 + MT128, 256, 0, stream>>>(Amat1, W1, M1, Amat2, W2, M2,
+                                               x0b, Bp1ext, Cp1, Nn);
+
+  combo_fold_ea1<<<FB_BLOCKS + (E + 255) / 256, 256, 0, stream>>>(M1, M2, Bcat1, RWcat,
+      ji, ii, etype, rowstart, prepos, Cp1, relb1, Matt1, recs1, E);
+
   agg1f<<<NB4, 256, 0, stream>>>(recs1, rowstart, x0b, XQ1, Nn);
   gemm_tile<1, 0, 1, 0><<<dim3(MT128, 4), 256, 0, stream>>>(XQ1, Bcat1, h1b, nullptr,
-      nullptr, nullptr, Nn, D2, 192, 768, 192, bias1, nullptr);
+      nullptr, nullptr, Nn, D2, KCAT, 768, KCAT, bias1, nullptr);
 
   gemm_tile<0, 0, 0, 1><<<dim3(MT128, 3), 256, 0, stream>>>(h1b, W2b, z2b, nullptr,
       Bp2ext, Cp2, Nn, OUTD, D2, D2, 0, nullptr, nullptr);
```
